# Optimization experiments

Measured on AMD Instinct MI355X. Metric: run time of the kernel, lower is better.

Reference implementation:

```python
import jax, jax.numpy as jnp
import numpy as np

HEADS = 8
DIM_HEAD = 64
SCALE = DIM_HEAD ** (-0.5)


def setup_inputs() -> dict:
    key = jax.random.key(0)
    ks = jax.random.split(key, 6)
    x = jax.random.normal(ks[0], (4, 2048, 1024), dtype=jnp.float32)
    context = jax.random.normal(ks[1], (4, 512, 768), dtype=jnp.float32)
    # linear weights stored as (in, out); init scaled like nn.Linear default-ish
    Wq = jax.random.normal(ks[2], (1024, 512), dtype=jnp.float32) * (1.0 / np.sqrt(1024))
    Wk = jax.random.normal(ks[3], (768, 512), dtype=jnp.float32) * (1.0 / np.sqrt(768))
    Wv = jax.random.normal(ks[4], (768, 512), dtype=jnp.float32) * (1.0 / np.sqrt(768))
    Wo = jax.random.normal(ks[5], (512, 1024), dtype=jnp.float32) * (1.0 / np.sqrt(512))
    return {"x": x, "context": context, "Wq": Wq, "Wk": Wk, "Wv": Wv, "Wo": Wo}


def reference(x, context, Wq, Wk, Wv, Wo):
    # projections: [b, i, inner], [b, j, inner]
    q = jnp.einsum('bid,de->bie', x, Wq)
    k = jnp.einsum('bjd,de->bje', context, Wk)
    v = jnp.einsum('bjd,de->bje', context, Wv)
    b, i, _ = q.shape
    j = k.shape[1]
    # split heads: [b, h, seq, c]
    q = q.reshape(b, i, HEADS, DIM_HEAD).transpose(0, 2, 1, 3)
    k = k.reshape(b, j, HEADS, DIM_HEAD).transpose(0, 2, 1, 3)
    v = v.reshape(b, j, HEADS, DIM_HEAD).transpose(0, 2, 1, 3)
    scores = jnp.einsum('bhic,bhjc->bhij', q, k) * SCALE
    attn = jax.nn.softmax(scores, axis=-1)
    out = jnp.einsum('bhij,bhjc->bhic', attn, v)  # [b, h, i, c]
    out = out.transpose(0, 2, 1, 3).reshape(b, i, HEADS * DIM_HEAD)
    return jnp.einsum('bie,ed->bid', out, Wo)
```

## Files before the change

### kernel.cpp

```cpp
#include <hip/hip_runtime.h>
#include <stdint.h>

typedef unsigned short u16;
typedef __attribute__((ext_vector_type(8))) short short8;
typedef __attribute__((ext_vector_type(4))) float f32x4;

#define MFMA16(a, b, c) __builtin_amdgcn_mfma_f32_16x16x32_bf16((a), (b), (c), 0, 0, 0)

__device__ __forceinline__ u16 f2bf(float f) {
  unsigned int u = __float_as_uint(f);
  u += 0x7FFFu + ((u >> 16) & 1u);
  return (u16)(u >> 16);
}

__device__ __forceinline__ void gload16(const u16* g, u16* lds) {
  __builtin_amdgcn_global_load_lds(
      (const __attribute__((address_space(1))) unsigned int*)g,
      (__attribute__((address_space(3))) unsigned int*)lds, 16, 0, 0);
}

__global__ void cvt_all(const float* __restrict__ x, u16* __restrict__ xb, int n4x,
                        const float* __restrict__ cx, u16* __restrict__ cb, int n4c) {
  int i = blockIdx.x * blockDim.x + threadIdx.x;
  int stride = gridDim.x * blockDim.x;
  int total = n4x + n4c;
  for (; i < total; i += stride) {
    float4 v = (i < n4x) ? ((const float4*)x)[i] : ((const float4*)cx)[i - n4x];
    ushort4 o;
    o.x = f2bf(v.x); o.y = f2bf(v.y); o.z = f2bf(v.z); o.w = f2bf(v.w);
    if (i < n4x) ((ushort4*)xb)[i] = o; else ((ushort4*)cb)[i - n4x] = o;
  }
}

__global__ void trans_all(const float* __restrict__ Wq, const float* __restrict__ Wk,
                          const float* __restrict__ Wv, const float* __restrict__ Wo,
                          u16* __restrict__ wqT, u16* __restrict__ wkvT,
                          u16* __restrict__ woT) {
  __shared__ float tile[32][33];
  int z = blockIdx.z;
  const float* src; u16* dst; int R, C; float scale = 1.0f;
  if (z == 0)      { src = Wq; dst = wqT;  R = 1024; C = 512;  scale = 0.125f; }
  else if (z == 1) { src = Wk; dst = wkvT; R = 768;  C = 512;  }
  else if (z == 2) { src = Wv; dst = wkvT + (size_t)512 * 768; R = 768; C = 512; }
  else             { src = Wo; dst = woT;  R = 512;  C = 1024; }
  int bx = blockIdx.x * 32, by = blockIdx.y * 32;
  if (bx >= C || by >= R) return;
  int tx = threadIdx.x, ty = threadIdx.y;
#pragma unroll
  for (int i = 0; i < 4; ++i)
    tile[ty + 8 * i][tx] = src[(size_t)(by + ty + 8 * i) * C + bx + tx];
  __syncthreads();
#pragma unroll
  for (int i = 0; i < 4; ++i)
    dst[(size_t)(bx + ty + 8 * i) * R + by + tx] = f2bf(tile[tx][ty + 8 * i] * scale);
}

template <int MODE>
__device__ __forceinline__ void gemm_body(const u16* __restrict__ A,
                                          const u16* __restrict__ BT,
                                          void* __restrict__ C0p,
                                          void* __restrict__ C1p,
                                          int tm, int tn, int K, int N, u16* smem) {
  u16* As = smem;
  u16* Bs = smem + 8192;
  const int t = threadIdx.x;
  const int w = t >> 6, l = t & 63, lr = l & 15, lg = l >> 4;
  const int wr = w >> 1, wc = w & 1;

  f32x4 acc[4][2];
#pragma unroll
  for (int mi = 0; mi < 4; ++mi)
#pragma unroll
    for (int ni = 0; ni < 2; ++ni) acc[mi][ni] = (f32x4){0.f, 0.f, 0.f, 0.f};

  for (int kt = 0; kt < K; kt += 64) {
#pragma unroll
    for (int p = 0; p < 4; ++p) {
      int idx = p * 256 + t, row = idx >> 3, cg = idx & 7;
      gload16(A + (size_t)(tm + row) * K + kt + ((cg ^ (row & 7)) * 8),
              As + (p * 256 + (t & 192)) * 8);
    }
#pragma unroll
    for (int pb = 0; pb < 2; ++pb) {
      int idx = pb * 256 + t, row = idx >> 3, cg = idx & 7;
      gload16(BT + (size_t)(tn + row) * K + kt + ((cg ^ (row & 7)) * 8),
              Bs + (pb * 256 + (t & 192)) * 8);
    }
    __syncthreads();
    short8 af[4][2], bf[2][2];
#pragma unroll
    for (int mi = 0; mi < 4; ++mi)
#pragma unroll
      for (int kk = 0; kk < 2; ++kk)
        af[mi][kk] = *(const short8*)
            &As[(wr * 64 + mi * 16 + lr) * 64 + (((kk * 4 + lg) ^ (lr & 7)) * 8)];
#pragma unroll
    for (int ni = 0; ni < 2; ++ni)
#pragma unroll
      for (int kk = 0; kk < 2; ++kk)
        bf[ni][kk] = *(const short8*)
            &Bs[(wc * 32 + ni * 16 + lr) * 64 + (((kk * 4 + lg) ^ (lr & 7)) * 8)];
#pragma unroll
    for (int mi = 0; mi < 4; ++mi)
#pragma unroll
      for (int ni = 0; ni < 2; ++ni) {
        acc[mi][ni] = MFMA16(af[mi][0], bf[ni][0], acc[mi][ni]);
        acc[mi][ni] = MFMA16(af[mi][1], bf[ni][1], acc[mi][ni]);
      }
    __syncthreads();
  }

  if (MODE == 2 && tn >= 512) {
    u16* tile = smem;
#pragma unroll
    for (int mi = 0; mi < 4; ++mi)
#pragma unroll
      for (int ni = 0; ni < 2; ++ni) {
        ushort4 pk;
        pk.x = f2bf(acc[mi][ni][0]); pk.y = f2bf(acc[mi][ni][1]);
        pk.z = f2bf(acc[mi][ni][2]); pk.w = f2bf(acc[mi][ni][3]);
        *(ushort4*)&tile[(wc * 32 + ni * 16 + lr) * 136 + wr * 64 + mi * 16 + lg * 4] = pk;
      }
    __syncthreads();
    int bh = ((tm >> 9) << 3) + ((tn - 512) >> 6);
    u16* dst = (u16*)C1p + (size_t)bh * 64 * 512 + (tm & 511);
#pragma unroll
    for (int p = 0; p < 4; ++p) {
      int c = (p * 256 + t) >> 4, jj = (t & 15) * 8;
      short8 v = *(const short8*)&tile[c * 136 + jj];
      *(short8*)(dst + (size_t)c * 512 + jj) = v;
    }
    return;
  }

#pragma unroll
  for (int mi = 0; mi < 4; ++mi)
#pragma unroll
    for (int ni = 0; ni < 2; ++ni)
#pragma unroll
      for (int r = 0; r < 4; ++r) {
        int rg = tm + wr * 64 + mi * 16 + lg * 4 + r;
        int cg = tn + wc * 32 + ni * 16 + lr;
        float val = acc[mi][ni][r];
        if (MODE == 0) {
          ((float*)C0p)[(size_t)rg * N + cg] = val;
        } else if (MODE == 1) {
          ((u16*)C0p)[(((size_t)(rg >> 11) * 8 + (cg >> 6)) * 2048 + (rg & 2047)) * 64 +
                      (cg & 63)] = f2bf(val);
        } else {
          ((u16*)C0p)[(((size_t)(rg >> 9) * 8 + (cg >> 6)) * 512 + (rg & 511)) * 64 +
                      (cg & 63)] = f2bf(val);
        }
      }
}

__global__ __launch_bounds__(256) void gemm_qkv(const u16* __restrict__ xb,
                                                const u16* __restrict__ wqT,
                                                u16* __restrict__ qhb,
                                                const u16* __restrict__ cb,
                                                const u16* __restrict__ wkvT,
                                                u16* __restrict__ khb,
                                                u16* __restrict__ vtb) {
  __shared__ __align__(16) u16 smem[12288];
  int gid = (int)blockIdx.x;
  gid = (gid & 7) * 96 + (gid >> 3);
  if (gid < 512) {
    gemm_body<1>(xb, wqT, qhb, nullptr, (gid >> 3) * 128, (gid & 7) * 64, 1024, 512, smem);
  } else {
    int g2 = gid - 512;
    gemm_body<2>(cb, wkvT, khb, vtb, (g2 >> 4) * 128, (g2 & 15) * 64, 768, 1024, smem);
  }
}

__global__ __launch_bounds__(256) void gemm_o(const u16* __restrict__ aob,
                                              const u16* __restrict__ woT,
                                              float* __restrict__ out) {
  __shared__ __align__(16) u16 smem[12288];
  int gid = (int)blockIdx.x;
  gid = (gid & 7) * 128 + (gid >> 3);
  gemm_body<0>(aob, woT, out, nullptr, (gid >> 4) * 128, (gid & 15) * 64, 512, 1024, smem);
}

__global__ __launch_bounds__(256) void attn_kernel(const u16* __restrict__ qhb,
                                                   const u16* __restrict__ khb,
                                                   const u16* __restrict__ vtb,
                                                   u16* __restrict__ aob) {
  __shared__ __align__(16) u16 kvb[2][128 * 64];
  __shared__ __align__(16) u16 pl[4][16 * 128];
  const int t = threadIdx.x, w = t >> 6, l = t & 63, i = l & 15, g = l >> 4;
  int lid = (int)blockIdx.x;
  lid = (lid & 7) * 128 + (lid >> 3);
  const int bh = lid >> 5, qt = lid & 31;
  const int i7 = i & 7;

  const u16* qp = qhb + ((size_t)bh * 2048 + qt * 64 + w * 16) * 64;
  const u16* kp = khb + (size_t)bh * 512 * 64;
  const u16* vp = vtb + (size_t)bh * 64 * 512;

  short8 qa0 = *(const short8*)(qp + (size_t)i * 64 + g * 8);
  short8 qa1 = *(const short8*)(qp + (size_t)i * 64 + 32 + g * 8);

  const int wbase = (t & 192) * 8;

#define STAGE_K(jq, buf)                                                      \
  {                                                                           \
    int R0 = (jq) * 128;                                                      \
    _Pragma("unroll") for (int p = 0; p < 4; ++p) {                           \
      int u = p * 256 + t;                                                    \
      int r = u >> 3;                                                         \
      int cc = ((u & 7) ^ (r & 7)) * 8;                                       \
      gload16(kp + (size_t)(R0 + r) * 64 + cc, kvb[buf] + p * 2048 + wbase);  \
    }                                                                         \
  }
#define STAGE_V(vq, buf)                                                      \
  {                                                                           \
    int J0 = (vq) * 128;                                                      \
    _Pragma("unroll") for (int p = 0; p < 4; ++p) {                           \
      int u = p * 256 + t;                                                    \
      int r = u >> 4;                                                         \
      int cc = ((u & 15) ^ (r & 7)) * 8;                                      \
      gload16(vp + (size_t)r * 512 + J0 + cc, kvb[buf] + p * 2048 + wbase);   \
    }                                                                         \
  }

  STAGE_K(0, 0);
  __syncthreads();

  f32x4 sc[32];
#pragma unroll
  for (int jq = 0; jq < 4; ++jq) {
    if (jq < 3) { STAGE_K(jq + 1, (jq + 1) & 1); }
    else        { STAGE_V(0, 0); }
    const u16* kb = kvb[jq & 1];
#pragma unroll
    for (int jt2 = 0; jt2 < 8; ++jt2) {
      int jt = jq * 8 + jt2;
      int r = jt2 * 16 + i;
      short8 k0 = *(const short8*)&kb[r * 64 + ((g ^ i7) * 8)];
      short8 k1 = *(const short8*)&kb[r * 64 + (((4 + g) ^ i7) * 8)];
      f32x4 a = (f32x4){0.f, 0.f, 0.f, 0.f};
      a = MFMA16(k0, qa0, a);
      a = MFMA16(k1, qa1, a);
      sc[jt] = a;
    }
    __syncthreads();
  }

  f32x4 vm = sc[0];
#pragma unroll
  for (int jt = 1; jt < 32; ++jt) {
#pragma unroll
    for (int r = 0; r < 4; ++r) vm[r] = fmaxf(vm[r], sc[jt][r]);
  }
  float mx = fmaxf(fmaxf(vm[0], vm[1]), fmaxf(vm[2], vm[3]));
  mx = fmaxf(mx, __shfl_xor(mx, 16));
  mx = fmaxf(mx, __shfl_xor(mx, 32));
  float sum = 0.f;
#pragma unroll
  for (int jt = 0; jt < 32; ++jt) {
#pragma unroll
    for (int r = 0; r < 4; ++r) {
      float e = __expf(sc[jt][r] - mx);
      sc[jt][r] = e;
      sum += e;
    }
  }
  sum += __shfl_xor(sum, 16);
  sum += __shfl_xor(sum, 32);
  float inv = 1.f / sum;

  u16* pw = pl[w];
  f32x4 oac[4];
#pragma unroll
  for (int ct = 0; ct < 4; ++ct) oac[ct] = (f32x4){0.f, 0.f, 0.f, 0.f};

#pragma unroll
  for (int vq = 0; vq < 4; ++vq) {
    if (vq < 3) { STAGE_V(vq + 1, (vq + 1) & 1); }
#pragma unroll
    for (int tt = 0; tt < 8; ++tt) {
      int jt = vq * 8 + tt;
      unsigned w0, w1;
      asm("v_cvt_pk_bf16_f32 %0, %1, %2" : "=v"(w0) : "v"(sc[jt][0]), "v"(sc[jt][1]));
      asm("v_cvt_pk_bf16_f32 %0, %1, %2" : "=v"(w1) : "v"(sc[jt][2]), "v"(sc[jt][3]));
      uint2 pk2; pk2.x = w0; pk2.y = w1;
      *(uint2*)&pw[i * 128 + ((tt * 16 + g * 4) ^ (i7 * 8))] = pk2;
    }
    asm volatile("s_waitcnt lgkmcnt(0)" ::: "memory");
    __builtin_amdgcn_sched_barrier(0);
    const u16* vb = kvb[vq & 1];
#pragma unroll
    for (int T = 0; T < 4; ++T) {
      short8 pa = *(const short8*)&pw[i * 128 + ((T * 32 + g * 8) ^ (i7 * 8))];
#pragma unroll
      for (int ct = 0; ct < 4; ++ct) {
        short8 vf = *(const short8*)&vb[(ct * 16 + i) * 128 + (((T * 4 + g) ^ i7) * 8)];
        oac[ct] = MFMA16(pa, vf, oac[ct]);
      }
    }
    __syncthreads();
  }

  float iv[4];
#pragma unroll
  for (int r = 0; r < 4; ++r) iv[r] = __shfl(inv, (l & 48) + g * 4 + r);
  u16* op = aob + ((size_t)(bh >> 3) * 2048 + qt * 64 + w * 16) * 512 + (bh & 7) * 64;
#pragma unroll
  for (int ct = 0; ct < 4; ++ct)
#pragma unroll
    for (int r = 0; r < 4; ++r)
      op[(size_t)(g * 4 + r) * 512 + ct * 16 + i] = f2bf(oac[ct][r] * iv[r]);
}

extern "C" void kernel_launch(void* const* d_in, const int* in_sizes, int n_in,
                              void* d_out, int out_size, void* d_ws, size_t ws_size,
                              hipStream_t stream) {
  const float* x  = (const float*)d_in[0];
  const float* cx = (const float*)d_in[1];
  const float* Wq = (const float*)d_in[2];
  const float* Wk = (const float*)d_in[3];
  const float* Wv = (const float*)d_in[4];
  const float* Wo = (const float*)d_in[5];
  float* out = (float*)d_out;

  char* p = (char*)d_ws;
  u16* xb   = (u16*)p; p += (size_t)8388608 * 2;
  u16* cb   = (u16*)p; p += (size_t)1572864 * 2;
  u16* wqT  = (u16*)p; p += (size_t)524288 * 2;
  u16* wkvT = (u16*)p; p += (size_t)786432 * 2;
  u16* woT  = (u16*)p; p += (size_t)524288 * 2;
  u16* qhb  = (u16*)p; p += (size_t)4194304 * 2;
  u16* khb  = (u16*)p; p += (size_t)1048576 * 2;
  u16* vtb  = (u16*)p; p += (size_t)1048576 * 2;
  u16* aob  = (u16*)p; p += (size_t)4194304 * 2;

  cvt_all<<<2048, 256, 0, stream>>>(x, xb, 8388608 / 4, cx, cb, 1572864 / 4);
  trans_all<<<dim3(32, 32, 4), dim3(32, 8), 0, stream>>>(Wq, Wk, Wv, Wo, wqT, wkvT, woT);

  gemm_qkv<<<768, 256, 0, stream>>>(xb, wqT, qhb, cb, wkvT, khb, vtb);
  attn_kernel<<<1024, 256, 0, stream>>>(qhb, khb, vtb, aob);
  gemm_o<<<1024, 256, 0, stream>>>(aob, woT, out);
}
```

Measured before the change: 79.79 us.

## Stage full K and V tiles in LDS at once instead of double-buffered chunks

```diff
diff --git a/kernel.cpp b/kernel.cpp
--- a/kernel.cpp
+++ b/kernel.cpp
@@ -185,7 +185,7 @@
                                                    const u16* __restrict__ khb,
                                                    const u16* __restrict__ vtb,
                                                    u16* __restrict__ aob) {
-  __shared__ __align__(16) u16 kvb[2][128 * 64];
+  __shared__ __align__(16) u16 kvb[512 * 64];
   __shared__ __align__(16) u16 pl[4][16 * 128];
   const int t = threadIdx.x, w = t >> 6, l = t & 63, i = l & 15, g = l >> 4;
   int lid = (int)blockIdx.x;
@@ -202,48 +202,32 @@
 
   const int wbase = (t & 192) * 8;
 
-#define STAGE_K(jq, buf)                                                      \
-  {                                                                           \
-    int R0 = (jq) * 128;                                                      \
-    _Pragma("unroll") for (int p = 0; p < 4; ++p) {                           \
-      int u = p * 256 + t;                                                    \
-      int r = u >> 3;                                                         \
-      int cc = ((u & 7) ^ (r & 7)) * 8;                                       \
-      gload16(kp + (size_t)(R0 + r) * 64 + cc, kvb[buf] + p * 2048 + wbase);  \
-    }                                                                         \
-  }
-#define STAGE_V(vq, buf)                                                      \
-  {                                                                           \
-    int J0 = (vq) * 128;                                                      \
-    _Pragma("unroll") for (int p = 0; p < 4; ++p) {                           \
-      int u = p * 256 + t;                                                    \
-      int r = u >> 4;                                                         \
-      int cc = ((u & 15) ^ (r & 7)) * 8;                                      \
-      gload16(vp + (size_t)r * 512 + J0 + cc, kvb[buf] + p * 2048 + wbase);   \
-    }                                                                         \
-  }
-
-  STAGE_K(0, 0);
+#pragma unroll
+  for (int p = 0; p < 16; ++p) {
+    int u = p * 256 + t;
+    int r = u >> 3, cg = u & 7;
+    gload16(kp + (size_t)r * 64 + ((cg ^ (r & 7)) * 8), kvb + p * 2048 + wbase);
+  }
   __syncthreads();
 
   f32x4 sc[32];
 #pragma unroll
-  for (int jq = 0; jq < 4; ++jq) {
-    if (jq < 3) { STAGE_K(jq + 1, (jq + 1) & 1); }
-    else        { STAGE_V(0, 0); }
-    const u16* kb = kvb[jq & 1];
-#pragma unroll
-    for (int jt2 = 0; jt2 < 8; ++jt2) {
-      int jt = jq * 8 + jt2;
-      int r = jt2 * 16 + i;
-      short8 k0 = *(const short8*)&kb[r * 64 + ((g ^ i7) * 8)];
-      short8 k1 = *(const short8*)&kb[r * 64 + (((4 + g) ^ i7) * 8)];
-      f32x4 a = (f32x4){0.f, 0.f, 0.f, 0.f};
-      a = MFMA16(k0, qa0, a);
-      a = MFMA16(k1, qa1, a);
-      sc[jt] = a;
-    }
-    __syncthreads();
+  for (int jt = 0; jt < 32; ++jt) {
+    int r = jt * 16 + i;
+    short8 k0 = *(const short8*)&kvb[r * 64 + ((g ^ i7) * 8)];
+    short8 k1 = *(const short8*)&kvb[r * 64 + (((4 + g) ^ i7) * 8)];
+    f32x4 a = (f32x4){0.f, 0.f, 0.f, 0.f};
+    a = MFMA16(k0, qa0, a);
+    a = MFMA16(k1, qa1, a);
+    sc[jt] = a;
+  }
+  __syncthreads();
+
+#pragma unroll
+  for (int p = 0; p < 16; ++p) {
+    int u = p * 256 + t;
+    int r = u >> 6, cg = u & 63;
+    gload16(vp + (size_t)r * 512 + ((cg ^ (r & 7)) * 8), kvb + p * 2048 + wbase);
   }
 
   f32x4 vm = sc[0];
@@ -269,17 +253,18 @@
   sum += __shfl_xor(sum, 32);
   float inv = 1.f / sum;
 
+  __syncthreads();
+
   u16* pw = pl[w];
   f32x4 oac[4];
 #pragma unroll
   for (int ct = 0; ct < 4; ++ct) oac[ct] = (f32x4){0.f, 0.f, 0.f, 0.f};
 
 #pragma unroll
-  for (int vq = 0; vq < 4; ++vq) {
-    if (vq < 3) { STAGE_V(vq + 1, (vq + 1) & 1); }
+  for (int c4 = 0; c4 < 4; ++c4) {
 #pragma unroll
     for (int tt = 0; tt < 8; ++tt) {
-      int jt = vq * 8 + tt;
+      int jt = c4 * 8 + tt;
       unsigned w0, w1;
       asm("v_cvt_pk_bf16_f32 %0, %1, %2" : "=v"(w0) : "v"(sc[jt][0]), "v"(sc[jt][1]));
       asm("v_cvt_pk_bf16_f32 %0, %1, %2" : "=v"(w1) : "v"(sc[jt][2]), "v"(sc[jt][3]));
@@ -288,17 +273,18 @@
     }
     asm volatile("s_waitcnt lgkmcnt(0)" ::: "memory");
     __builtin_amdgcn_sched_barrier(0);
-    const u16* vb = kvb[vq & 1];
-#pragma unroll
-    for (int T = 0; T < 4; ++T) {
-      short8 pa = *(const short8*)&pw[i * 128 + ((T * 32 + g * 8) ^ (i7 * 8))];
+#pragma unroll
+    for (int T2 = 0; T2 < 4; ++T2) {
+      short8 pa = *(const short8*)&pw[i * 128 + ((T2 * 32 + g * 8) ^ (i7 * 8))];
+      int jg = c4 * 16 + T2 * 4 + g;
 #pragma unroll
       for (int ct = 0; ct < 4; ++ct) {
-        short8 vf = *(const short8*)&vb[(ct * 16 + i) * 128 + (((T * 4 + g) ^ i7) * 8)];
+        int vr = ct * 16 + i;
+        short8 vf = *(const short8*)&kvb[vr * 512 + ((jg ^ (vr & 7)) * 8)];
         oac[ct] = MFMA16(pa, vf, oac[ct]);
       }
     }
-    __syncthreads();
+    asm volatile("" ::: "memory");
   }
 
   float iv[4];
```

Measured after the change: 75.70 us. 5.1% less time.
